# Kernel optimization log

Hardware: AMD Instinct MI355X
Metric: run time of the kernel (lower is better)

The kernel has to match this reference:

```python
import jax, jax.numpy as jnp
import numpy as np

N = 16_777_216  # number of draft tokens / cache slots
ACCEPT_PROB = 0.7


def setup_inputs() -> dict:
    key = jax.random.key(0)
    k1, k2, k3 = jax.random.split(key, 3)
    idx = jax.random.randint(k1, (N,), 0, N, dtype=jnp.int64)
    keep = jax.random.uniform(k2, (N,)) < ACCEPT_PROB
    # rejected slots are marked -1, as in the original kernel
    accept_index = jnp.where(keep, idx, jnp.int64(-1))
    out_cache_loc = jax.random.normal(k3, (N,), dtype=jnp.float32)
    return {"accept_index": accept_index, "out_cache_loc": out_cache_loc}


def reference(accept_index, out_cache_loc):
    """Stream compaction: gather out_cache_loc[accept_index[i]] for every i with
    accept_index[i] >= 0, packed densely at the front of the output.

    The original returns an array of length num_accepted (data-dependent). For a
    static, jit-compatible shape we return a length-N array whose first
    num_accepted entries equal the original output and the rest are zero.
    """
    n = accept_index.shape[0]
    mask = accept_index >= 0                      # [N] bool
    # exclusive prefix sum of mask = destination slot for each accepted element
    dst = jnp.cumsum(mask.astype(jnp.int64)) - mask.astype(jnp.int64)  # [N]
    # gather (use 0 as a safe dummy index for rejected lanes)
    vals = out_cache_loc[jnp.where(mask, accept_index, 0)]             # [N]
    # scatter accepted values to their compacted slots; rejected lanes are
    # routed to index n, which mode='drop' discards
    scatter_idx = jnp.where(mask, dst, n)
    out = jnp.zeros((n,), dtype=out_cache_loc.dtype)
    out = out.at[scatter_idx].set(vals, mode="drop")
    return out
```

## Files before the change

kernel.cpp:

```cpp
#include <hip/hip_runtime.h>


#define N_TOTAL  16777216
#define BLOCK    256

#define EPT      16
#define TILE     (BLOCK * EPT)
#define NBLOCKS  (N_TOTAL / TILE)

#define EPT2     32
#define TILE2    (BLOCK * EPT2)
#define NB2      (N_TOTAL / TILE2)

#define SLICE_LG 22
#define SLICES   (N_TOTAL >> SLICE_LG)

typedef float vfloat4 __attribute__((ext_vector_type(4)));

__global__ __launch_bounds__(BLOCK) void k_reduce(const int* __restrict__ idx,
                                                  int* __restrict__ blockSums) {
    const int b = blockIdx.x;
    const int t = threadIdx.x;
    const int4* p = (const int4*)(idx + (size_t)b * TILE + (size_t)t * EPT);
    int cnt = 0;
#pragma unroll
    for (int j = 0; j < EPT / 4; ++j) {
        int4 v = p[j];
        cnt += (v.x >= 0) + (v.y >= 0) + (v.z >= 0) + (v.w >= 0);
    }
#pragma unroll
    for (int d = 32; d > 0; d >>= 1) cnt += __shfl_down(cnt, d);
    __shared__ int wsum[BLOCK / 64];
    const int lane = t & 63, wave = t >> 6;
    if (lane == 0) wsum[wave] = cnt;
    __syncthreads();
    if (t == 0) {
        int s = 0;
#pragma unroll
        for (int w = 0; w < BLOCK / 64; ++w) s += wsum[w];
        blockSums[b] = s;
    }
}

__global__ __launch_bounds__(256) void k_scan(const int* __restrict__ blockSums,
                                              int* __restrict__ blockOffsets) {
    const int t = threadIdx.x;
    const int lane = t & 63, wave = t >> 6;
    int vals[16];
    const int4* p = (const int4*)(blockSums + t * 16);
#pragma unroll
    for (int j = 0; j < 4; ++j) {
        int4 v = p[j];
        vals[4 * j + 0] = v.x; vals[4 * j + 1] = v.y;
        vals[4 * j + 2] = v.z; vals[4 * j + 3] = v.w;
    }
    int tsum = 0;
#pragma unroll
    for (int j = 0; j < 16; ++j) tsum += vals[j];

    int x = tsum;
#pragma unroll
    for (int d = 1; d < 64; d <<= 1) {
        int y = __shfl_up(x, d);
        if (lane >= d) x += y;
    }
    __shared__ int wsum[4], woff[4];
    if (lane == 63) wsum[wave] = x;
    __syncthreads();
    if (t == 0) {
        int s = 0;
#pragma unroll
        for (int w = 0; w < 4; ++w) { woff[w] = s; s += wsum[w]; }
        blockOffsets[NBLOCKS] = s;
    }
    __syncthreads();
    int run = (x - tsum) + woff[wave];
#pragma unroll
    for (int j = 0; j < 16; ++j) {
        blockOffsets[t * 16 + j] = run;
        run += vals[j];
    }
}

__global__ __launch_bounds__(BLOCK) void k_scatter(const int* __restrict__ idx,
                                                   const float* __restrict__ src,
                                                   const int* __restrict__ blockOffsets,
                                                   float* __restrict__ out) {
    const int b = blockIdx.x;
    const int t = threadIdx.x;
    const int lane = t & 63, wave = t >> 6;
    const int4* p = (const int4*)(idx + (size_t)b * TILE2 + (size_t)t * EPT2);
    int v[EPT2];
#pragma unroll
    for (int j = 0; j < EPT2 / 4; ++j) {
        int4 q = p[j];
        v[4 * j + 0] = q.x; v[4 * j + 1] = q.y;
        v[4 * j + 2] = q.z; v[4 * j + 3] = q.w;
    }

    int cnt = 0;
#pragma unroll
    for (int j = 0; j < EPT2; ++j) cnt += (v[j] >= 0);

    int x = cnt;
#pragma unroll
    for (int d = 1; d < 64; d <<= 1) {
        int y = __shfl_up(x, d);
        if (lane >= d) x += y;
    }
    __shared__ int wsum[BLOCK / 64], woff[BLOCK / 64];
    __shared__ int btotal;
    if (lane == 63) wsum[wave] = x;
    __syncthreads();
    if (t == 0) {
        int s = 0;
#pragma unroll
        for (int w = 0; w < BLOCK / 64; ++w) { woff[w] = s; s += wsum[w]; }
        btotal = s;
    }
    __syncthreads();
    const int off0 = (x - cnt) + woff[wave];

    __shared__ float vals[TILE2];
#pragma unroll 1
    for (int s = 0; s < SLICES; ++s) {
        float tmp[EPT2];
#pragma unroll
        for (int j = 0; j < EPT2; ++j) {
            const bool m = (int)((unsigned)v[j] >> SLICE_LG) == s;
            tmp[j] = src[m ? v[j] : 0];
        }
        asm volatile("s_waitcnt vmcnt(0)" ::: "memory");
        int o = off0;
#pragma unroll
        for (int j = 0; j < EPT2; ++j) {
            const bool acc = v[j] >= 0;
            const bool m = (int)((unsigned)v[j] >> SLICE_LG) == s;
            if (m) vals[o] = tmp[j];
            o += acc;
        }
    }
    __syncthreads();

    const int base = blockOffsets[2 * b];
    const int tot  = btotal;
    for (int i = t; i < tot; i += BLOCK)
        __builtin_nontemporal_store(vals[i], out + base + i);
}

__global__ __launch_bounds__(256) void k_tail(float* __restrict__ out,
                                              const int* __restrict__ total_p) {
    const int total = *total_p;
    const int i = (blockIdx.x * 256 + threadIdx.x) * 4;
    if (i >= total) {
        vfloat4 z = (vfloat4)(0.f);
        __builtin_nontemporal_store(z, (vfloat4*)(out + i));
    } else if (i + 4 > total) {
#pragma unroll
        for (int k = 0; k < 4; ++k)
            if (i + k >= total) out[i + k] = 0.f;
    }
}

extern "C" void kernel_launch(void* const* d_in, const int* in_sizes, int n_in,
                              void* d_out, int out_size, void* d_ws, size_t ws_size,
                              hipStream_t stream) {
    const int*   idx = (const int*)d_in[0];
    const float* src = (const float*)d_in[1];
    float*       out = (float*)d_out;

    int* blockSums    = (int*)d_ws;
    int* blockOffsets = blockSums + NBLOCKS;

    k_reduce <<<NBLOCKS, BLOCK, 0, stream>>>(idx, blockSums);
    k_scan   <<<1, 256, 0, stream>>>(blockSums, blockOffsets);
    k_scatter<<<NB2, BLOCK, 0, stream>>>(idx, src, blockOffsets, out);
    k_tail   <<<N_TOTAL / 4 / 256, 256, 0, stream>>>(out, blockOffsets + NBLOCKS);
}
```

Baseline: 342.7 us.

## Bin gather indices by source slice to localize random reads

Replaces the slice-looped gather with a multi-pass pipeline. Indices are counted and binned by 4MB source slice and written to a workspace buffer. The gather then reads the binned indices slice by slice, with blocks arranged so that each slice stays resident in cache, and the emit pass reads the results back in original order and compacts them. The aim is to cut random-access DRAM traffic to src, at the cost of several extra full streaming passes, extra workspace, and shared-memory atomics. The old path remains as a fallback when the workspace is too small.

```diff
diff --git a/kernel.cpp b/kernel.cpp
--- a/kernel.cpp
+++ b/kernel.cpp
@@ -3,147 +3,323 @@
 
 #define N_TOTAL  16777216
 #define BLOCK    256
+#define EPT2     32
+#define TILE2    (BLOCK * EPT2)
+#define NB2      (N_TOTAL / TILE2)
+#define SLICE_LG 20
+#define SLICES   16
 
 #define EPT      16
 #define TILE     (BLOCK * EPT)
 #define NBLOCKS  (N_TOTAL / TILE)
-
-#define EPT2     32
-#define TILE2    (BLOCK * EPT2)
-#define NB2      (N_TOTAL / TILE2)
-
-#define SLICE_LG 22
-#define SLICES   (N_TOTAL >> SLICE_LG)
+#define SLICE_LG5 22
+#define SLICES5  (N_TOTAL >> SLICE_LG5)
 
 typedef float vfloat4 __attribute__((ext_vector_type(4)));
 
-__global__ __launch_bounds__(BLOCK) void k_reduce(const int* __restrict__ idx,
-                                                  int* __restrict__ blockSums) {
-    const int b = blockIdx.x;
-    const int t = threadIdx.x;
-    const int4* p = (const int4*)(idx + (size_t)b * TILE + (size_t)t * EPT);
-    int cnt = 0;
-#pragma unroll
-    for (int j = 0; j < EPT / 4; ++j) {
-        int4 v = p[j];
-        cnt += (v.x >= 0) + (v.y >= 0) + (v.z >= 0) + (v.w >= 0);
-    }
-#pragma unroll
-    for (int d = 32; d > 0; d >>= 1) cnt += __shfl_down(cnt, d);
-    __shared__ int wsum[BLOCK / 64];
-    const int lane = t & 63, wave = t >> 6;
-    if (lane == 0) wsum[wave] = cnt;
-    __syncthreads();
-    if (t == 0) {
-        int s = 0;
-#pragma unroll
-        for (int w = 0; w < BLOCK / 64; ++w) s += wsum[w];
-        blockSums[b] = s;
-    }
-}
-
-__global__ __launch_bounds__(256) void k_scan(const int* __restrict__ blockSums,
-                                              int* __restrict__ blockOffsets) {
-    const int t = threadIdx.x;
-    const int lane = t & 63, wave = t >> 6;
-    int vals[16];
-    const int4* p = (const int4*)(blockSums + t * 16);
-#pragma unroll
-    for (int j = 0; j < 4; ++j) {
-        int4 v = p[j];
-        vals[4 * j + 0] = v.x; vals[4 * j + 1] = v.y;
-        vals[4 * j + 2] = v.z; vals[4 * j + 3] = v.w;
-    }
-    int tsum = 0;
-#pragma unroll
-    for (int j = 0; j < 16; ++j) tsum += vals[j];
-
-    int x = tsum;
-#pragma unroll
-    for (int d = 1; d < 64; d <<= 1) {
-        int y = __shfl_up(x, d);
-        if (lane >= d) x += y;
-    }
-    __shared__ int wsum[4], woff[4];
-    if (lane == 63) wsum[wave] = x;
-    __syncthreads();
-    if (t == 0) {
-        int s = 0;
-#pragma unroll
-        for (int w = 0; w < 4; ++w) { woff[w] = s; s += wsum[w]; }
-        blockOffsets[NBLOCKS] = s;
-    }
-    __syncthreads();
-    int run = (x - tsum) + woff[wave];
-#pragma unroll
-    for (int j = 0; j < 16; ++j) {
-        blockOffsets[t * 16 + j] = run;
-        run += vals[j];
-    }
-}
-
-__global__ __launch_bounds__(BLOCK) void k_scatter(const int* __restrict__ idx,
-                                                   const float* __restrict__ src,
-                                                   const int* __restrict__ blockOffsets,
-                                                   float* __restrict__ out) {
-    const int b = blockIdx.x;
-    const int t = threadIdx.x;
-    const int lane = t & 63, wave = t >> 6;
+__global__ __launch_bounds__(BLOCK) void k_count(const int* __restrict__ idx,
+                                                 int* __restrict__ cnt) {
+    __shared__ int h[SLICES];
+    const int b = blockIdx.x, t = threadIdx.x;
+    if (t < SLICES) h[t] = 0;
+    __syncthreads();
     const int4* p = (const int4*)(idx + (size_t)b * TILE2 + (size_t)t * EPT2);
     int v[EPT2];
 #pragma unroll
     for (int j = 0; j < EPT2 / 4; ++j) {
         int4 q = p[j];
-        v[4 * j + 0] = q.x; v[4 * j + 1] = q.y;
-        v[4 * j + 2] = q.z; v[4 * j + 3] = q.w;
-    }
-
+        v[4*j+0]=q.x; v[4*j+1]=q.y; v[4*j+2]=q.z; v[4*j+3]=q.w;
+    }
+#pragma unroll
+    for (int j = 0; j < EPT2; ++j) {
+        unsigned s = (unsigned)v[j] >> SLICE_LG;
+        if (s < SLICES) atomicAdd(&h[s], 1);
+    }
+    __syncthreads();
+    if (t < SLICES) cnt[b * SLICES + t] = h[t];
+}
+
+__global__ __launch_bounds__(BLOCK) void k_scan2(const int* __restrict__ cnt,
+                                                 int* __restrict__ off,
+                                                 int* __restrict__ sliceBase,
+                                                 int* __restrict__ blockOff) {
+    const int t = threadIdx.x, lane = t & 63, wave = t >> 6;
+    const int R = NB2 / BLOCK;
+    int sum[SLICES];
+#pragma unroll
+    for (int s = 0; s < SLICES; ++s) sum[s] = 0;
+    for (int r = 0; r < R; ++r) {
+        const int4* row = (const int4*)(cnt + (size_t)(t * R + r) * SLICES);
+        int4 c0 = row[0], c1 = row[1], c2 = row[2], c3 = row[3];
+        sum[0]+=c0.x; sum[1]+=c0.y; sum[2]+=c0.z; sum[3]+=c0.w;
+        sum[4]+=c1.x; sum[5]+=c1.y; sum[6]+=c1.z; sum[7]+=c1.w;
+        sum[8]+=c2.x; sum[9]+=c2.y; sum[10]+=c2.z; sum[11]+=c2.w;
+        sum[12]+=c3.x; sum[13]+=c3.y; sum[14]+=c3.z; sum[15]+=c3.w;
+    }
+    int inc[SLICES];
+#pragma unroll
+    for (int s = 0; s < SLICES; ++s) inc[s] = sum[s];
+#pragma unroll
+    for (int d = 1; d < 64; d <<= 1) {
+#pragma unroll
+        for (int s = 0; s < SLICES; ++s) {
+            int u = __shfl_up(inc[s], d);
+            if (lane >= d) inc[s] += u;
+        }
+    }
+    int tTot = 0;
+#pragma unroll
+    for (int s = 0; s < SLICES; ++s) tTot += sum[s];
+    int tInc = tTot;
+#pragma unroll
+    for (int d = 1; d < 64; d <<= 1) {
+        int u = __shfl_up(tInc, d);
+        if (lane >= d) tInc += u;
+    }
+    __shared__ int wtot[4][SLICES], wstot[4];
+    __shared__ int wbase[4][SLICES], wsbase[4];
+    if (lane == 63) {
+#pragma unroll
+        for (int s = 0; s < SLICES; ++s) wtot[wave][s] = inc[s];
+        wstot[wave] = tInc;
+    }
+    __syncthreads();
+    if (t == 0) {
+        int run[SLICES];
+#pragma unroll
+        for (int s = 0; s < SLICES; ++s) run[s] = 0;
+        for (int w = 0; w < 4; ++w)
+#pragma unroll
+            for (int s = 0; s < SLICES; ++s) { wbase[w][s] = run[s]; run[s] += wtot[w][s]; }
+        int sr = 0;
+#pragma unroll
+        for (int s = 0; s < SLICES; ++s) { sliceBase[s] = sr; sr += run[s]; }
+        sliceBase[SLICES] = sr;
+        blockOff[NB2] = sr;
+        int rs = 0;
+        for (int w = 0; w < 4; ++w) { wsbase[w] = rs; rs += wstot[w]; }
+    }
+    __syncthreads();
+    int ex[SLICES];
+#pragma unroll
+    for (int s = 0; s < SLICES; ++s) ex[s] = inc[s] - sum[s] + wbase[wave][s];
+    int exA = tInc - tTot + wsbase[wave];
+    for (int r = 0; r < R; ++r) {
+        const int b = t * R + r;
+        blockOff[b] = exA;
+        const int4* row = (const int4*)(cnt + (size_t)b * SLICES);
+        int4 c0 = row[0], c1 = row[1], c2 = row[2], c3 = row[3];
+        int rv[SLICES] = {c0.x,c0.y,c0.z,c0.w, c1.x,c1.y,c1.z,c1.w,
+                          c2.x,c2.y,c2.z,c2.w, c3.x,c3.y,c3.z,c3.w};
+#pragma unroll
+        for (int s = 0; s < SLICES; ++s) {
+            off[(size_t)b * SLICES + s] = ex[s];
+            ex[s] += rv[s];
+            exA   += rv[s];
+        }
+    }
+}
+
+__global__ __launch_bounds__(BLOCK) void k_bin(const int* __restrict__ idx,
+                                               const int* __restrict__ off,
+                                               const int* __restrict__ sliceBase,
+                                               int* __restrict__ bins) {
+    const int b = blockIdx.x, t = threadIdx.x, lane = t & 63, wave = t >> 6;
+    const int4* p = (const int4*)(idx + (size_t)b * TILE2 + (size_t)t * EPT2);
+    int v[EPT2];
+#pragma unroll
+    for (int j = 0; j < EPT2 / 4; ++j) {
+        int4 q = p[j];
+        v[4*j+0]=q.x; v[4*j+1]=q.y; v[4*j+2]=q.z; v[4*j+3]=q.w;
+    }
+    int tc[SLICES];
+#pragma unroll
+    for (int s = 0; s < SLICES; ++s) tc[s] = 0;
+#pragma unroll
+    for (int j = 0; j < EPT2; ++j) {
+        unsigned s = (unsigned)v[j] >> SLICE_LG;
+#pragma unroll
+        for (int s2 = 0; s2 < SLICES; ++s2) tc[s2] += (s == (unsigned)s2);
+    }
+    int inc[SLICES];
+#pragma unroll
+    for (int s = 0; s < SLICES; ++s) inc[s] = tc[s];
+#pragma unroll
+    for (int d = 1; d < 64; d <<= 1) {
+#pragma unroll
+        for (int s = 0; s < SLICES; ++s) {
+            int u = __shfl_up(inc[s], d);
+            if (lane >= d) inc[s] += u;
+        }
+    }
+    __shared__ int wtot[4][SLICES], wbase[4][SLICES];
+    __shared__ int gbase[SLICES], segStart[SLICES + 1];
+    if (lane == 63)
+#pragma unroll
+        for (int s = 0; s < SLICES; ++s) wtot[wave][s] = inc[s];
+    __syncthreads();
+    if (t == 0) {
+        int run[SLICES];
+#pragma unroll
+        for (int s = 0; s < SLICES; ++s) run[s] = 0;
+        for (int w = 0; w < 4; ++w)
+#pragma unroll
+            for (int s = 0; s < SLICES; ++s) { wbase[w][s] = run[s]; run[s] += wtot[w][s]; }
+        int sr = 0;
+#pragma unroll
+        for (int s = 0; s < SLICES; ++s) { segStart[s] = sr; sr += run[s]; }
+        segStart[SLICES] = sr;
+#pragma unroll
+        for (int s = 0; s < SLICES; ++s)
+            gbase[s] = sliceBase[s] + off[(size_t)b * SLICES + s] - segStart[s];
+    }
+    __syncthreads();
+    __shared__ int exb[BLOCK][SLICES + 1];
+    __shared__ int binsBuf[TILE2];
+#pragma unroll
+    for (int s = 0; s < SLICES; ++s)
+        exb[t][s] = segStart[s] + (inc[s] - tc[s]) + wbase[wave][s];
+#pragma unroll
+    for (int j = 0; j < EPT2; ++j) {
+        unsigned s = (unsigned)v[j] >> SLICE_LG;
+        if (s < SLICES) {
+            int pLoc = exb[t][s]++;
+            binsBuf[pLoc] = v[j];
+        }
+    }
+    __syncthreads();
+    const int tot = segStart[SLICES];
+    for (int k = t; k < tot; k += BLOCK) {
+        int x = binsBuf[k];
+        int s = 0;
+#pragma unroll
+        for (int q = 1; q < SLICES; ++q) s += (k >= segStart[q]);
+        __builtin_nontemporal_store(x, bins + gbase[s] + k);
+    }
+}
+
+__global__ __launch_bounds__(BLOCK) void k_gather(const int* __restrict__ bins,
+                                                  const float* __restrict__ src,
+                                                  const int* __restrict__ sliceBase,
+                                                  float* __restrict__ val) {
+    __shared__ int pad[18432];
+    const int t = threadIdx.x;
+    pad[t] = t;
+    const int n = blockIdx.x;
+    const int x = n & 7;
+    const int g = n >> 9;
+    const int q = (n >> 3) & 63;
+    const int s = 2 * x + (g >> 1);
+    const int c = (g & 1) * 64 + q;
+    const int s0 = sliceBase[s], s1 = sliceBase[s + 1];
+    if (s1 == -1) val[0] = (float)pad[t];
+    const int len = s1 - s0;
+    const int L = (len + 127) >> 7;
+    const int start = s0 + c * L;
+    const int end = (start + L < s1) ? (start + L) : s1;
+    for (int k0 = start + t; k0 < end; k0 += BLOCK * 8) {
+        int kk[8], bm[8];
+        float fm[8];
+#pragma unroll
+        for (int m = 0; m < 8; ++m) kk[m] = k0 + m * BLOCK;
+#pragma unroll
+        for (int m = 0; m < 8; ++m) {
+            int kc = kk[m] < end ? kk[m] : end - 1;
+            bm[m] = __builtin_nontemporal_load(bins + kc);
+        }
+#pragma unroll
+        for (int m = 0; m < 8; ++m) fm[m] = src[bm[m]];
+#pragma unroll
+        for (int m = 0; m < 8; ++m)
+            if (kk[m] < end) __builtin_nontemporal_store(fm[m], val + kk[m]);
+    }
+}
+
+__global__ __launch_bounds__(BLOCK) void k_emit(const int* __restrict__ idx,
+                                                const int* __restrict__ off,
+                                                const int* __restrict__ sliceBase,
+                                                const int* __restrict__ blockOff,
+                                                const float* __restrict__ val,
+                                                float* __restrict__ out) {
+    const int b = blockIdx.x, t = threadIdx.x, lane = t & 63, wave = t >> 6;
+    const int4* p = (const int4*)(idx + (size_t)b * TILE2 + (size_t)t * EPT2);
+    int v[EPT2];
+#pragma unroll
+    for (int j = 0; j < EPT2 / 4; ++j) {
+        int4 q = p[j];
+        v[4*j+0]=q.x; v[4*j+1]=q.y; v[4*j+2]=q.z; v[4*j+3]=q.w;
+    }
+    int tc[SLICES];
+#pragma unroll
+    for (int s = 0; s < SLICES; ++s) tc[s] = 0;
+#pragma unroll
+    for (int j = 0; j < EPT2; ++j) {
+        unsigned s = (unsigned)v[j] >> SLICE_LG;
+#pragma unroll
+        for (int s2 = 0; s2 < SLICES; ++s2) tc[s2] += (s == (unsigned)s2);
+    }
+    int inc[SLICES];
+#pragma unroll
+    for (int s = 0; s < SLICES; ++s) inc[s] = tc[s];
+#pragma unroll
+    for (int d = 1; d < 64; d <<= 1) {
+#pragma unroll
+        for (int s = 0; s < SLICES; ++s) {
+            int u = __shfl_up(inc[s], d);
+            if (lane >= d) inc[s] += u;
+        }
+    }
     int cnt = 0;
 #pragma unroll
-    for (int j = 0; j < EPT2; ++j) cnt += (v[j] >= 0);
-
-    int x = cnt;
-#pragma unroll
-    for (int d = 1; d < 64; d <<= 1) {
-        int y = __shfl_up(x, d);
-        if (lane >= d) x += y;
-    }
-    __shared__ int wsum[BLOCK / 64], woff[BLOCK / 64];
-    __shared__ int btotal;
-    if (lane == 63) wsum[wave] = x;
-    __syncthreads();
-    if (t == 0) {
-        int s = 0;
-#pragma unroll
-        for (int w = 0; w < BLOCK / 64; ++w) { woff[w] = s; s += wsum[w]; }
-        btotal = s;
-    }
-    __syncthreads();
-    const int off0 = (x - cnt) + woff[wave];
-
+    for (int s = 0; s < SLICES; ++s) cnt += tc[s];
+    int xinc = cnt;
+#pragma unroll
+    for (int d = 1; d < 64; d <<= 1) {
+        int u = __shfl_up(xinc, d);
+        if (lane >= d) xinc += u;
+    }
+    __shared__ int wtot[4][SLICES], wbase[4][SLICES];
+    __shared__ int wsum[4], woff[4], sTot;
+    if (lane == 63) {
+#pragma unroll
+        for (int s = 0; s < SLICES; ++s) wtot[wave][s] = inc[s];
+        wsum[wave] = xinc;
+    }
+    __syncthreads();
+    if (t == 0) {
+        int run[SLICES];
+#pragma unroll
+        for (int s = 0; s < SLICES; ++s) run[s] = 0;
+        for (int w = 0; w < 4; ++w)
+#pragma unroll
+            for (int s = 0; s < SLICES; ++s) { wbase[w][s] = run[s]; run[s] += wtot[w][s]; }
+        int rs = 0;
+        for (int w = 0; w < 4; ++w) { woff[w] = rs; rs += wsum[w]; }
+        sTot = rs;
+    }
+    __syncthreads();
+    __shared__ int exb[BLOCK][SLICES + 1];
+#pragma unroll
+    for (int s = 0; s < SLICES; ++s)
+        exb[t][s] = sliceBase[s] + off[(size_t)b * SLICES + s]
+                  + (inc[s] - tc[s]) + wbase[wave][s];
+    int slotA[EPT2];
+#pragma unroll
+    for (int j = 0; j < EPT2; ++j) {
+        unsigned s = (unsigned)v[j] >> SLICE_LG;
+        slotA[j] = (s < SLICES) ? exb[t][s]++ : 0;
+    }
+    float tmp[EPT2];
+#pragma unroll
+    for (int j = 0; j < EPT2; ++j) tmp[j] = val[slotA[j]];
     __shared__ float vals[TILE2];
-#pragma unroll 1
-    for (int s = 0; s < SLICES; ++s) {
-        float tmp[EPT2];
-#pragma unroll
-        for (int j = 0; j < EPT2; ++j) {
-            const bool m = (int)((unsigned)v[j] >> SLICE_LG) == s;
-            tmp[j] = src[m ? v[j] : 0];
-        }
-        asm volatile("s_waitcnt vmcnt(0)" ::: "memory");
-        int o = off0;
-#pragma unroll
-        for (int j = 0; j < EPT2; ++j) {
-            const bool acc = v[j] >= 0;
-            const bool m = (int)((unsigned)v[j] >> SLICE_LG) == s;
-            if (m) vals[o] = tmp[j];
-            o += acc;
-        }
-    }
-    __syncthreads();
-
-    const int base = blockOffsets[2 * b];
-    const int tot  = btotal;
+    int o = (xinc - cnt) + woff[wave];
+#pragma unroll
+    for (int j = 0; j < EPT2; ++j)
+        if (v[j] >= 0) vals[o++] = tmp[j];
+    __syncthreads();
+    const int base = blockOff[b];
+    const int tot = sTot;
     for (int i = t; i < tot; i += BLOCK)
         __builtin_nontemporal_store(vals[i], out + base + i);
 }
@@ -162,6 +338,128 @@
     }
 }
 
+__global__ __launch_bounds__(BLOCK) void k_reduce(const int* __restrict__ idx,
+                                                  int* __restrict__ blockSums) {
+    const int b = blockIdx.x, t = threadIdx.x;
+    const int4* p = (const int4*)(idx + (size_t)b * TILE + (size_t)t * EPT);
+    int cnt = 0;
+#pragma unroll
+    for (int j = 0; j < EPT / 4; ++j) {
+        int4 v = p[j];
+        cnt += (v.x >= 0) + (v.y >= 0) + (v.z >= 0) + (v.w >= 0);
+    }
+#pragma unroll
+    for (int d = 32; d > 0; d >>= 1) cnt += __shfl_down(cnt, d);
+    __shared__ int wsum[BLOCK / 64];
+    const int lane = t & 63, wave = t >> 6;
+    if (lane == 0) wsum[wave] = cnt;
+    __syncthreads();
+    if (t == 0) {
+        int s = 0;
+#pragma unroll
+        for (int w = 0; w < BLOCK / 64; ++w) s += wsum[w];
+        blockSums[b] = s;
+    }
+}
+
+__global__ __launch_bounds__(256) void k_scan(const int* __restrict__ blockSums,
+                                              int* __restrict__ blockOffsets) {
+    const int t = threadIdx.x;
+    const int lane = t & 63, wave = t >> 6;
+    int vals[16];
+    const int4* p = (const int4*)(blockSums + t * 16);
+#pragma unroll
+    for (int j = 0; j < 4; ++j) {
+        int4 v = p[j];
+        vals[4*j+0]=v.x; vals[4*j+1]=v.y; vals[4*j+2]=v.z; vals[4*j+3]=v.w;
+    }
+    int tsum = 0;
+#pragma unroll
+    for (int j = 0; j < 16; ++j) tsum += vals[j];
+    int x = tsum;
+#pragma unroll
+    for (int d = 1; d < 64; d <<= 1) {
+        int y = __shfl_up(x, d);
+        if (lane >= d) x += y;
+    }
+    __shared__ int wsum[4], woff[4];
+    if (lane == 63) wsum[wave] = x;
+    __syncthreads();
+    if (t == 0) {
+        int s = 0;
+#pragma unroll
+        for (int w = 0; w < 4; ++w) { woff[w] = s; s += wsum[w]; }
+        blockOffsets[NBLOCKS] = s;
+    }
+    __syncthreads();
+    int run = (x - tsum) + woff[wave];
+#pragma unroll
+    for (int j = 0; j < 16; ++j) {
+        blockOffsets[t * 16 + j] = run;
+        run += vals[j];
+    }
+}
+
+__global__ __launch_bounds__(BLOCK) void k_scatter(const int* __restrict__ idx,
+                                                   const float* __restrict__ src,
+                                                   const int* __restrict__ blockOffsets,
+                                                   float* __restrict__ out) {
+    const int b = blockIdx.x, t = threadIdx.x;
+    const int lane = t & 63, wave = t >> 6;
+    const int4* p = (const int4*)(idx + (size_t)b * TILE2 + (size_t)t * EPT2);
+    int v[EPT2];
+#pragma unroll
+    for (int j = 0; j < EPT2 / 4; ++j) {
+        int4 q = p[j];
+        v[4*j+0]=q.x; v[4*j+1]=q.y; v[4*j+2]=q.z; v[4*j+3]=q.w;
+    }
+    int cnt = 0;
+#pragma unroll
+    for (int j = 0; j < EPT2; ++j) cnt += (v[j] >= 0);
+    int x = cnt;
+#pragma unroll
+    for (int d = 1; d < 64; d <<= 1) {
+        int y = __shfl_up(x, d);
+        if (lane >= d) x += y;
+    }
+    __shared__ int wsum[BLOCK / 64], woff[BLOCK / 64];
+    __shared__ int btotal;
+    if (lane == 63) wsum[wave] = x;
+    __syncthreads();
+    if (t == 0) {
+        int s = 0;
+#pragma unroll
+        for (int w = 0; w < BLOCK / 64; ++w) { woff[w] = s; s += wsum[w]; }
+        btotal = s;
+    }
+    __syncthreads();
+    const int off0 = (x - cnt) + woff[wave];
+    __shared__ float vals[TILE2];
+#pragma unroll 1
+    for (int s = 0; s < SLICES5; ++s) {
+        float tmp[EPT2];
+#pragma unroll
+        for (int j = 0; j < EPT2; ++j) {
+            const bool m = (int)((unsigned)v[j] >> SLICE_LG5) == s;
+            tmp[j] = src[m ? v[j] : 0];
+        }
+        asm volatile("s_waitcnt vmcnt(0)" ::: "memory");
+        int o = off0;
+#pragma unroll
+        for (int j = 0; j < EPT2; ++j) {
+            const bool acc = v[j] >= 0;
+            const bool m = (int)((unsigned)v[j] >> SLICE_LG5) == s;
+            if (m) vals[o] = tmp[j];
+            o += acc;
+        }
+    }
+    __syncthreads();
+    const int base = blockOffsets[2 * b];
+    const int tot  = btotal;
+    for (int i = t; i < tot; i += BLOCK)
+        __builtin_nontemporal_store(vals[i], out + base + i);
+}
+
 extern "C" void kernel_launch(void* const* d_in, const int* in_sizes, int n_in,
                               void* d_out, int out_size, void* d_ws, size_t ws_size,
                               hipStream_t stream) {
@@ -169,11 +467,28 @@
     const float* src = (const float*)d_in[1];
     float*       out = (float*)d_out;
 
-    int* blockSums    = (int*)d_ws;
-    int* blockOffsets = blockSums + NBLOCKS;
-
-    k_reduce <<<NBLOCKS, BLOCK, 0, stream>>>(idx, blockSums);
-    k_scan   <<<1, 256, 0, stream>>>(blockSums, blockOffsets);
-    k_scatter<<<NB2, BLOCK, 0, stream>>>(idx, src, blockOffsets, out);
-    k_tail   <<<N_TOTAL / 4 / 256, 256, 0, stream>>>(out, blockOffsets + NBLOCKS);
-}
+    int* cnt       = (int*)d_ws;
+    int* off       = cnt + NB2 * SLICES;
+    int* sliceBase = off + NB2 * SLICES;
+    int* blockOff  = sliceBase + (SLICES + 1);
+    int* bins      = blockOff + (NB2 + 1);
+    float* val     = (float*)(bins + N_TOTAL);
+    const size_t need = ((size_t)(2 * NB2 * SLICES + SLICES + 1 + NB2 + 1)
+                         + 2ull * N_TOTAL) * 4ull;
+
+    if (ws_size >= need) {
+        k_count <<<NB2, BLOCK, 0, stream>>>(idx, cnt);
+        k_scan2 <<<1, BLOCK, 0, stream>>>(cnt, off, sliceBase, blockOff);
+        k_bin   <<<NB2, BLOCK, 0, stream>>>(idx, off, sliceBase, bins);
+        k_gather<<<NB2, BLOCK, 0, stream>>>(bins, src, sliceBase, val);
+        k_emit  <<<NB2, BLOCK, 0, stream>>>(idx, off, sliceBase, blockOff, val, out);
+        k_tail  <<<N_TOTAL / 4 / 256, 256, 0, stream>>>(out, blockOff + NB2);
+    } else {
+        int* blockSums    = (int*)d_ws;
+        int* blockOffsets = blockSums + NBLOCKS;
+        k_reduce <<<NBLOCKS, BLOCK, 0, stream>>>(idx, blockSums);
+        k_scan   <<<1, 256, 0, stream>>>(blockSums, blockOffsets);
+        k_scatter<<<NB2, BLOCK, 0, stream>>>(idx, src, blockOffsets, out);
+        k_tail   <<<N_TOTAL / 4 / 256, 256, 0, stream>>>(out, blockOffsets + NBLOCKS);
+    }
+}
```

Result: slower. 369.2 us (+7.7%).
